# Kernel tuning notes

Measured on AMD Instinct MI355X. Metric: run time of the kernel, lower is better.

The kernel has to match this reference:

```python
import jax, jax.numpy as jnp
import numpy as np
import math

B, N, D, H, O = 2, 1024, 256, 4, 8
DT, STEPS = 0.1, 5


def setup_inputs() -> dict:
    key = jax.random.key(0)
    ks = jax.random.split(key, 8)
    inv_d = 1.0 / math.sqrt(D)
    inv_ho = 1.0 / math.sqrt(H * O)
    return {
        "x": jax.random.normal(ks[0], (B, N, D), jnp.float32),
        "Wq": jax.random.normal(ks[1], (D, D), jnp.float32) * inv_d,
        "Wk": jax.random.normal(ks[2], (D, D), jnp.float32) * inv_d,
        "Wp": jax.random.normal(ks[3], (H * O, D), jnp.float32) * inv_d,
        "bp": jnp.zeros((H * O,), jnp.float32),
        "Wo": jax.random.normal(ks[4], (D, H * O), jnp.float32) * inv_ho,
        "bo": jnp.zeros((D,), jnp.float32),
        "omega": jax.random.normal(ks[5], (H, O), jnp.float32) * 0.1,
        "coupling_scale": jnp.asarray(1.0, jnp.float32),
    }


def reference(x, Wq, Wk, Wp, bp, Wo, bo, omega, coupling_scale):
    dk = D // H
    # attention coupling J_ij = softmax(q_i.k_j / sqrt(d_k))  -> (B,H,N,N)
    q = (x @ Wq.T).reshape(B, N, H, dk).transpose(0, 2, 1, 3)
    k = (x @ Wk.T).reshape(B, N, H, dk).transpose(0, 2, 1, 3)
    J = jax.nn.softmax(jnp.einsum('bhid,bhjd->bhij', q, k) / math.sqrt(dk), axis=-1)
    # initial phases (B,H,N,O)
    phases = (x @ Wp.T + bp).reshape(B, N, H, O).transpose(0, 2, 1, 3)
    om = omega[None, :, None, :]  # (1,H,1,O)

    def step(ph, _):
        # sum_j J_ij sin(phi_j - phi_i) = cos(phi_i)*(J@sin phi) - sin(phi_i)*(J@cos phi)
        s, c = jnp.sin(ph), jnp.cos(ph)
        coupling = c * jnp.einsum('bhij,bhjo->bhio', J, s) - s * jnp.einsum('bhij,bhjo->bhio', J, c)
        new = ph + DT * (om + coupling_scale * coupling)
        new = jnp.remainder(new + jnp.pi, 2 * jnp.pi) - jnp.pi
        return new, None

    phases, _ = jax.lax.scan(step, phases, None, length=STEPS)
    sig = jnp.cos(phases).transpose(0, 2, 1, 3).reshape(B, N, H * O)
    return sig @ Wo.T + bo
```

## Files before the change

kernel.cpp:

```cpp
#include <hip/hip_runtime.h>
#include <hip/hip_bf16.h>
#include <math.h>


#define NB 1024
#define NH 4
#define DD 256
#define NO 8
#define SCSZ 131072
#define PI_F      3.14159265358979323846f
#define TWO_PI_F  6.28318530717958647692f
#define INV_2PI_F 0.15915494309189533577f

typedef __attribute__((ext_vector_type(8))) short bf16x8;
typedef __attribute__((ext_vector_type(4))) float f32x4;
typedef unsigned long long u64;

__device__ __forceinline__ float b2f_u(unsigned short s) {
    union { unsigned u; float f; } x; x.u = ((unsigned)s) << 16; return x.f;
}
__device__ __forceinline__ unsigned short f2b(float f) {
    union { float f; unsigned u; } v; v.f = f;
    unsigned r = v.u + 0x7FFFu + ((v.u >> 16) & 1u);
    return (unsigned short)(r >> 16);
}
template<bool F32>
__device__ __forceinline__ uint4 load_pack8(const void* p, size_t off) {
    if (!F32) return *(const uint4*)((const unsigned short*)p + off);
    const float* fp = (const float*)p + off;
    float4 a = *(const float4*)fp;
    float4 b = *(const float4*)(fp + 4);
    uint4 r;
    r.x = (unsigned)f2b(a.x) | ((unsigned)f2b(a.y) << 16);
    r.y = (unsigned)f2b(a.z) | ((unsigned)f2b(a.w) << 16);
    r.z = (unsigned)f2b(b.x) | ((unsigned)f2b(b.y) << 16);
    r.w = (unsigned)f2b(b.z) | ((unsigned)f2b(b.w) << 16);
    return r;
}
__device__ __forceinline__ void load8_rt(int f32, const void* p, int i, float* f) {
    if (f32) {
        const float* fp = (const float*)p + i;
        float4 a = *(const float4*)fp;
        float4 b = *(const float4*)(fp + 4);
        f[0]=a.x; f[1]=a.y; f[2]=a.z; f[3]=a.w;
        f[4]=b.x; f[5]=b.y; f[6]=b.z; f[7]=b.w;
    } else {
        uint4 u = *(const uint4*)((const unsigned short*)p + i);
        f[0] = b2f_u(u.x & 0xFFFFu); f[1] = b2f_u(u.x >> 16);
        f[2] = b2f_u(u.y & 0xFFFFu); f[3] = b2f_u(u.y >> 16);
        f[4] = b2f_u(u.z & 0xFFFFu); f[5] = b2f_u(u.z >> 16);
        f[6] = b2f_u(u.w & 0xFFFFu); f[7] = b2f_u(u.w >> 16);
    }
}
__device__ __forceinline__ float read_cs_bf16(const void* p) {
    float vb = b2f_u(*(const unsigned short*)p);
    bool ok = isfinite(vb) && fabsf(vb) > 1e-30f && fabsf(vb) < 1e30f;
    if (ok) return vb;
    return *(const float*)p;
}
__device__ __forceinline__ int detect_inline(const unsigned short* x) {
    int l = threadIdx.x & 63;
    float a0 = fabsf(b2f_u(x[2 * l]));
    float a1 = fabsf(b2f_u(x[2 * (l + 64)]));
    unsigned long long b0 = __ballot(!(a0 >= 1e-10f && a0 <= 100.0f));
    unsigned long long b1 = __ballot(!(a1 >= 1e-10f && a1 <= 100.0f));
    return (__popcll(b0) + __popcll(b1)) > 16;
}
__device__ __forceinline__ void st8_llc(void* p, u64 v) {
    __hip_atomic_store((u64*)p, v, __ATOMIC_RELAXED, __HIP_MEMORY_SCOPE_AGENT);
}
__device__ __forceinline__ void wait_ctr(unsigned int* c, unsigned target) {
    unsigned spins = 0;
    while (__hip_atomic_load(c, __ATOMIC_RELAXED, __HIP_MEMORY_SCOPE_AGENT) < target) {
        __builtin_amdgcn_s_sleep(8);
        if (++spins > (1u << 18)) break;
    }
}

template<bool F32>
__device__ void projm_impl(
    const void* __restrict__ x, const void* __restrict__ Wq,
    const void* __restrict__ Wk, const void* __restrict__ Wp,
    const void* __restrict__ bp,
    unsigned short* __restrict__ Qb, unsigned short* __restrict__ Kb,
    float* __restrict__ PH, unsigned short* __restrict__ SC)
{
    __shared__ uint4 Xsh[64 * 32];
    __shared__ uint4 Wsh[64 * 32];
    const int tid = threadIdx.x;
    const int ftile = blockIdx.x % 9, itile = blockIdx.x / 9;
    const int i0 = itile * 64, f0 = ftile * 64;
    const int wave = tid >> 6, lane = tid & 63;
    const int n = lane & 15, quad = lane >> 4;

    #pragma unroll
    for (int g = 0; g < 8; g++) {
        int fidx = g * 256 + tid;
        int row = fidx >> 5, q = fidx & 31;
        int sw = (q & 24) | ((q ^ row) & 7);
        Xsh[row * 32 + sw] = load_pack8<F32>(x, (size_t)(i0 + row) * 256 + q * 8);
        int wr = f0 + row;
        uint4 wv = make_uint4(0, 0, 0, 0);
        if (wr < 256)      wv = load_pack8<F32>(Wq, (size_t)wr * 256 + q * 8);
        else if (wr < 512) wv = load_pack8<F32>(Wk, (size_t)(wr - 256) * 256 + q * 8);
        else if (wr < 544) wv = load_pack8<F32>(Wp, (size_t)(wr - 512) * 256 + q * 8);
        Wsh[row * 32 + sw] = wv;
    }
    __syncthreads();

    f32x4 acc[4];
    #pragma unroll
    for (int s = 0; s < 4; s++) acc[s] = (f32x4){0.f, 0.f, 0.f, 0.f};
    const int xrow = wave * 16 + n;
    #pragma unroll
    for (int s = 0; s < 8; s++) {
        int qc = s * 4 + quad;
        bf16x8 b = ((const bf16x8*)Xsh)[xrow * 32 + ((qc & 24) | ((qc ^ xrow) & 7))];
        #pragma unroll
        for (int sub = 0; sub < 4; sub++) {
            int wr = sub * 16 + n;
            bf16x8 a = ((const bf16x8*)Wsh)[wr * 32 + ((qc & 24) | ((qc ^ wr) & 7))];
            acc[sub] = __builtin_amdgcn_mfma_f32_16x16x32_bf16(a, b, acc[sub], 0, 0, 0);
        }
    }

    const int ig = i0 + wave * 16 + n;
    const int bb = ig >> 10, nr = ig & 1023;
    if (ftile < 4) {
        #pragma unroll
        for (int sub = 0; sub < 4; sub++) {
            int dd = sub * 16 + quad * 4;
            ushort4 v = make_ushort4(f2b(acc[sub][0] * 0.125f), f2b(acc[sub][1] * 0.125f),
                                     f2b(acc[sub][2] * 0.125f), f2b(acc[sub][3] * 0.125f));
            *(ushort4*)(Qb + ((size_t)((bb * NH + ftile) * NB + nr)) * 64 + dd) = v;
        }
    } else if (ftile < 8) {
        int h = ftile - 4;
        #pragma unroll
        for (int sub = 0; sub < 4; sub++) {
            int dd = sub * 16 + quad * 4;
            ushort4 v = make_ushort4(f2b(acc[sub][0]), f2b(acc[sub][1]),
                                     f2b(acc[sub][2]), f2b(acc[sub][3]));
            *(ushort4*)(Kb + ((size_t)((bb * NH + h) * NB + nr)) * 64 + dd) = v;
        }
    } else {
        #pragma unroll
        for (int sub = 0; sub < 2; sub++) {
            #pragma unroll
            for (int r = 0; r < 4; r++) {
                int fp = sub * 16 + quad * 4 + r;
                int h2 = fp >> 3, o = fp & 7;
                float bpv = F32 ? ((const float*)bp)[fp]
                                : b2f_u(((const unsigned short*)bp)[fp]);
                float v = acc[sub][r] + bpv;
                int bh = bb * NH + h2;
                PH[(size_t)bh * 8192 + o * 1024 + nr] = v;
                float sv, cv;
                __sincosf(v, &sv, &cv);
                SC[(size_t)(bh * 16 + o) * 1024 + nr]     = f2b(sv);
                SC[(size_t)(bh * 16 + 8 + o) * 1024 + nr] = f2b(cv);
            }
        }
    }
}

__global__ __launch_bounds__(256) void k_projm(
    const unsigned short* x, const void* Wq, const void* Wk, const void* Wp,
    const void* bp, unsigned short* Qb, unsigned short* Kb, float* PH,
    unsigned short* SC, unsigned int* ctr)
{
    if (blockIdx.x == 0) {
        #pragma unroll
        for (int i = 0; i < 5; i++) ctr[threadIdx.x + 256 * i] = 0u;
    }
    if (detect_inline(x)) projm_impl<true >(x, Wq, Wk, Wp, bp, Qb, Kb, PH, SC);
    else                  projm_impl<false>(x, Wq, Wk, Wp, bp, Qb, Kb, PH, SC);
}

__global__ __launch_bounds__(256) void k_mega4(
    const unsigned short* __restrict__ xraw,
    const unsigned short* __restrict__ Qb, const unsigned short* __restrict__ Kb,
    const float* __restrict__ PH0,
    unsigned short* __restrict__ SCB,
    const void* __restrict__ omega, const void* __restrict__ csp,
    const void* __restrict__ Wo, const void* __restrict__ bo,
    void* __restrict__ out, unsigned int* __restrict__ ctr)
{
    __shared__ uint4 Ush[16 * 128];
    __shared__ f32x4 red[4][64];
    __shared__ float redS[4][16];
    __shared__ float Rsh[16];
    __shared__ float sig[4][32];

    const int tid = threadIdx.x;
    const int bid = blockIdx.x;
    const int bh  = bid >> 6;
    const int i0  = (bid & 63) * 16;
    const int wave = tid >> 6, lane = tid & 63;
    const int n = lane & 15, quad = lane >> 4;
    const int f32 = detect_inline(xraw);

    const unsigned short* qrow = Qb + ((size_t)(bh * NB) + i0 + n) * 64;
    bf16x8 bq0 = *(const bf16x8*)(qrow + quad * 8);
    bf16x8 bq1 = *(const bf16x8*)(qrow + 32 + quad * 8);
    float s = 0.f;
    const unsigned short* kbase = Kb + ((size_t)(bh * NB) + n) * 64;
    #pragma unroll
    for (int t = 0; t < 16; t++) {
        int jt = wave * 16 + t;
        const unsigned short* arow = kbase + (size_t)jt * 16 * 64;
        bf16x8 a0 = *(const bf16x8*)(arow + quad * 8);
        bf16x8 a1 = *(const bf16x8*)(arow + 32 + quad * 8);
        f32x4 acc = {0.f, 0.f, 0.f, 0.f};
        acc = __builtin_amdgcn_mfma_f32_16x16x32_bf16(a0, bq0, acc, 0, 0, 0);
        acc = __builtin_amdgcn_mfma_f32_16x16x32_bf16(a1, bq1, acc, 0, 0, 0);
        float u0 = __expf(acc[0]);
        float u1 = __expf(acc[1]);
        float u2 = __expf(acc[2]);
        float u3 = __expf(acc[3]);
        s += (u0 + u1) + (u2 + u3);
        ushort4 uv = make_ushort4(f2b(u0), f2b(u1), f2b(u2), f2b(u3));
        int cw = 2 * jt + (quad >> 1);
        ((ushort4*)Ush)[(n * 128 + (cw ^ (n & 7))) * 2 + (quad & 1)] = uv;
    }
    s += __shfl_xor(s, 16);
    s += __shfl_xor(s, 32);
    if (lane < 16) redS[wave][lane] = s;
    __syncthreads();
    if (tid < 16)
        Rsh[tid] = 1.0f / (redS[0][tid] + redS[1][tid] + redS[2][tid] + redS[3][tid]);

    float P[4];
    float cs_ = 0.f, om_ = 0.f;
    if (wave == 0 && n < 8) {
        const int o = n, h = bh & 3;
        cs_ = f32 ? *(const float*)csp : read_cs_bf16(csp);
        om_ = f32 ? ((const float*)omega)[h * NO + o]
                  : b2f_u(((const unsigned short*)omega)[h * NO + o]);
        float4 pv = *(const float4*)(PH0 + (size_t)bh * 8192 + o * 1024 + i0 + quad * 4);
        P[0] = pv.x; P[1] = pv.y; P[2] = pv.z; P[3] = pv.w;
    }

    #pragma unroll 1
    for (int k = 0; k < 5; k++) {
        const unsigned short* scrow = SCB + (size_t)k * SCSZ + (size_t)(bh * 16 + n) * 1024;
        unsigned short* scout       = SCB + (size_t)(k + 1) * SCSZ;
        f32x4 acc = {0.f, 0.f, 0.f, 0.f};
        #pragma unroll
        for (int t = 0; t < 8; t++) {
            int it = wave * 8 + t;
            bf16x8 a = ((const bf16x8*)Ush)[n * 128 + ((it * 4 + quad) ^ (n & 7))];
            bf16x8 b = *(const bf16x8*)(scrow + it * 32 + quad * 8);
            acc = __builtin_amdgcn_mfma_f32_16x16x32_bf16(a, b, acc, 0, 0, 0);
        }
        red[wave][lane] = acc;
        __syncthreads();

        if (wave == 0) {
            f32x4 a0 = red[0][lane], a1 = red[1][lane];
            f32x4 a2 = red[2][lane], a3 = red[3][lane];
            #pragma unroll
            for (int v = 0; v < 4; v++) acc[v] = (a0[v] + a1[v]) + (a2[v] + a3[v]);
            float C0 = __shfl_xor(acc[0], 8);
            float C1 = __shfl_xor(acc[1], 8);
            float C2 = __shfl_xor(acc[2], 8);
            float C3 = __shfl_xor(acc[3], 8);
            if (n < 8) {
                const int o = n;
                float S[4] = {acc[0], acc[1], acc[2], acc[3]};
                float C[4] = {C0, C1, C2, C3};
                float Rr[4] = {Rsh[quad * 4], Rsh[quad * 4 + 1],
                               Rsh[quad * 4 + 2], Rsh[quad * 4 + 3]};
                unsigned short sb[4], cb[4];
                #pragma unroll
                for (int r = 0; r < 4; r++) {
                    float si, ci;
                    __sincosf(P[r], &si, &ci);
                    float coup = (ci * S[r] - si * C[r]) * Rr[r];
                    float v = P[r] + 0.1f * (om_ + cs_ * coup);
                    float t2 = v + PI_F;
                    t2 -= floorf(t2 * INV_2PI_F) * TWO_PI_F;
                    P[r] = t2 - PI_F;
                    float sn, cn;
                    __sincosf(P[r], &sn, &cn);
                    sb[r] = f2b(sn); cb[r] = f2b(cn);
                }
                u64 sv = (u64)sb[0] | ((u64)sb[1] << 16) | ((u64)sb[2] << 32) | ((u64)sb[3] << 48);
                u64 cv = (u64)cb[0] | ((u64)cb[1] << 16) | ((u64)cb[2] << 32) | ((u64)cb[3] << 48);
                int i = i0 + quad * 4;
                st8_llc(scout + (size_t)(bh * 16 + o) * 1024 + i,     sv);
                st8_llc(scout + (size_t)(bh * 16 + 8 + o) * 1024 + i, cv);
            }
        }
        __syncthreads();
        if (tid == 0) {
            unsigned int* c = &ctr[(k * 8 + bh) * 32];
            atomicAdd(c, 1u);
            if (k < 4) wait_ctr(c, 64u);
        }
        if (k == 4 && tid < 4) {
            int ob = bid >> 8;
            wait_ctr(&ctr[(4 * 8 + (ob * NH + tid)) * 32], 64u);
        }
        __syncthreads();
    }

    const unsigned short* scfin = SCB + (size_t)5 * SCSZ;
    const int ob = bid >> 8, n0 = (bid & 255) * 4;
    if (tid < 32) {
        int h = tid >> 3, o = tid & 7;
        u64 q = *(const u64*)(scfin + (size_t)((ob * NH + h) * 16 + 8 + o) * 1024 + n0);
        #pragma unroll
        for (int r = 0; r < 4; r++)
            sig[r][tid] = b2f_u((unsigned short)(q >> (16 * r)));
    }
    __syncthreads();
    float wv[32];
    #pragma unroll
    for (int d0 = 0; d0 < 32; d0 += 8) load8_rt(f32, Wo, tid * 32 + d0, wv + d0);
    const float bov = f32 ? ((const float*)bo)[tid] : b2f_u(((const unsigned short*)bo)[tid]);
    #pragma unroll
    for (int r = 0; r < 4; r++) {
        float acc = bov;
        #pragma unroll
        for (int t = 0; t < 32; t++) acc += sig[r][t] * wv[t];
        size_t oi = ((size_t)ob * 1024 + n0 + r) * DD + tid;
        if (f32) ((float*)out)[oi] = acc;
        else     ((unsigned short*)out)[oi] = f2b(acc);
    }
}

extern "C" void kernel_launch(void* const* d_in, const int* in_sizes, int n_in,
                              void* d_out, int out_size, void* d_ws, size_t ws_size,
                              hipStream_t stream)
{
    const unsigned short* x = (const unsigned short*)d_in[0];
    const void* Wq  = d_in[1];
    const void* Wk  = d_in[2];
    const void* Wp  = d_in[3];
    const void* bp  = d_in[4];
    const void* Wo  = d_in[5];
    const void* bo  = d_in[6];
    const void* om  = d_in[7];
    const void* cs  = d_in[8];

    char* w = (char*)d_ws;
    unsigned short* Qb  = (unsigned short*)w;
    unsigned short* Kb  = (unsigned short*)(w + (1u << 20));
    float*          PH0 = (float*)(w + (2u << 20));
    unsigned short* SCB = (unsigned short*)(w + (2u << 20) + (256u << 10));
    unsigned int*   ctr = (unsigned int*)(w + (4u << 20));

    k_projm<<<288, 256, 0, stream>>>(x, Wq, Wk, Wp, bp, Qb, Kb, PH0, SCB, ctr);
    k_mega4<<<512, 256, 0, stream>>>(x, Qb, Kb, PH0, SCB, om, cs,
                                     Wo, bo, d_out, ctr);
}
```

Before: 122.2 us.

## Replace counter barriers with per-data flag polling on nonzero bf16 values

Removes the per-step atomic counter grid barrier. Consumers instead poll the sin/cos buffer slots directly until they become nonzero. Producers force every bf16 value to be nonzero so zero can mean 'not yet written', and the projection kernel zeroes the later step buffers up front. Each block then waits only on the exact data it needs rather than on all 64 blocks, at the cost of extra zeroing traffic, a tiny perturbation of exact-zero values, and reliance on relaxed-ordering visibility of 8-byte stores.

```diff
diff --git a/kernel.cpp b/kernel.cpp
--- a/kernel.cpp
+++ b/kernel.cpp
@@ -23,6 +23,11 @@
     union { float f; unsigned u; } v; v.f = f;
     unsigned r = v.u + 0x7FFFu + ((v.u >> 16) & 1u);
     return (unsigned short)(r >> 16);
+}
+__device__ __forceinline__ unsigned short f2b_nz(float f) {
+    unsigned short u = f2b(f);
+    if ((u & 0x7FFFu) == 0u) u |= 1u;
+    return u;
 }
 template<bool F32>
 __device__ __forceinline__ uint4 load_pack8(const void* p, size_t off) {
@@ -69,12 +74,21 @@
 __device__ __forceinline__ void st8_llc(void* p, u64 v) {
     __hip_atomic_store((u64*)p, v, __ATOMIC_RELAXED, __HIP_MEMORY_SCOPE_AGENT);
 }
-__device__ __forceinline__ void wait_ctr(unsigned int* c, unsigned target) {
-    unsigned spins = 0;
-    while (__hip_atomic_load(c, __ATOMIC_RELAXED, __HIP_MEMORY_SCOPE_AGENT) < target) {
-        __builtin_amdgcn_s_sleep(8);
-        if (++spins > (1u << 18)) break;
-    }
+__device__ __forceinline__ u64 poll_g(const void* p) {
+    u64 g; unsigned spins = 0;
+    for (;;) {
+        g = __hip_atomic_load((const u64*)p, __ATOMIC_RELAXED,
+                              __HIP_MEMORY_SCOPE_AGENT);
+        if (g) break;
+        __builtin_amdgcn_s_sleep(1);
+        if (++spins > (1u << 17)) break;
+    }
+    return g;
+}
+__device__ __forceinline__ void barrier_lds() {
+    asm volatile("s_waitcnt lgkmcnt(0)" ::: "memory");
+    __builtin_amdgcn_s_barrier();
+    __builtin_amdgcn_sched_barrier(0);
 }
 
 template<bool F32>
@@ -157,8 +171,8 @@
                 PH[(size_t)bh * 8192 + o * 1024 + nr] = v;
                 float sv, cv;
                 __sincosf(v, &sv, &cv);
-                SC[(size_t)(bh * 16 + o) * 1024 + nr]     = f2b(sv);
-                SC[(size_t)(bh * 16 + 8 + o) * 1024 + nr] = f2b(cv);
+                SC[(size_t)(bh * 16 + o) * 1024 + nr]     = f2b_nz(sv);
+                SC[(size_t)(bh * 16 + 8 + o) * 1024 + nr] = f2b_nz(cv);
             }
         }
     }
@@ -167,11 +181,13 @@
 __global__ __launch_bounds__(256) void k_projm(
     const unsigned short* x, const void* Wq, const void* Wk, const void* Wp,
     const void* bp, unsigned short* Qb, unsigned short* Kb, float* PH,
-    unsigned short* SC, unsigned int* ctr)
+    unsigned short* SC)
 {
-    if (blockIdx.x == 0) {
-        #pragma unroll
-        for (int i = 0; i < 5; i++) ctr[threadIdx.x + 256 * i] = 0u;
+    {
+        uint4* zb = (uint4*)(SC + SCSZ);
+        const unsigned stride = gridDim.x * 256u;
+        for (unsigned idx = blockIdx.x * 256u + threadIdx.x; idx < 81920u; idx += stride)
+            zb[idx] = make_uint4(0u, 0u, 0u, 0u);
     }
     if (detect_inline(x)) projm_impl<true >(x, Wq, Wk, Wp, bp, Qb, Kb, PH, SC);
     else                  projm_impl<false>(x, Wq, Wk, Wp, bp, Qb, Kb, PH, SC);
@@ -184,7 +200,7 @@
     unsigned short* __restrict__ SCB,
     const void* __restrict__ omega, const void* __restrict__ csp,
     const void* __restrict__ Wo, const void* __restrict__ bo,
-    void* __restrict__ out, unsigned int* __restrict__ ctr)
+    void* __restrict__ out)
 {
     __shared__ uint4 Ush[16 * 128];
     __shared__ f32x4 red[4][64];
@@ -245,16 +261,48 @@
     for (int k = 0; k < 5; k++) {
         const unsigned short* scrow = SCB + (size_t)k * SCSZ + (size_t)(bh * 16 + n) * 1024;
         unsigned short* scout       = SCB + (size_t)(k + 1) * SCSZ;
+
+        uint4 f[8];
+        #pragma unroll
+        for (int t = 0; t < 8; t++)
+            f[t] = *(const uint4*)(scrow + (wave * 8 + t) * 32 + quad * 8);
+
+        {
+            unsigned spins = 0;
+            for (;;) {
+                unsigned pending = 0;
+                #pragma unroll
+                for (int t = 0; t < 8; t++) {
+                    const unsigned short* fp = scrow + (wave * 8 + t) * 32 + quad * 8;
+                    if ((f[t].x | f[t].y) == 0u) {
+                        u64 g = __hip_atomic_load((const u64*)fp, __ATOMIC_RELAXED,
+                                                  __HIP_MEMORY_SCOPE_AGENT);
+                        f[t].x = (unsigned)g; f[t].y = (unsigned)(g >> 32);
+                        if (g == 0) pending = 1u;
+                    }
+                    if ((f[t].z | f[t].w) == 0u) {
+                        u64 g = __hip_atomic_load((const u64*)(fp + 4), __ATOMIC_RELAXED,
+                                                  __HIP_MEMORY_SCOPE_AGENT);
+                        f[t].z = (unsigned)g; f[t].w = (unsigned)(g >> 32);
+                        if (g == 0) pending = 1u;
+                    }
+                }
+                if (!pending) break;
+                __builtin_amdgcn_s_sleep(1);
+                if (++spins > (1u << 17)) break;
+            }
+        }
+
         f32x4 acc = {0.f, 0.f, 0.f, 0.f};
         #pragma unroll
         for (int t = 0; t < 8; t++) {
             int it = wave * 8 + t;
             bf16x8 a = ((const bf16x8*)Ush)[n * 128 + ((it * 4 + quad) ^ (n & 7))];
-            bf16x8 b = *(const bf16x8*)(scrow + it * 32 + quad * 8);
-            acc = __builtin_amdgcn_mfma_f32_16x16x32_bf16(a, b, acc, 0, 0, 0);
+            union { uint4 u; bf16x8 b; } cvt; cvt.u = f[t];
+            acc = __builtin_amdgcn_mfma_f32_16x16x32_bf16(a, cvt.b, acc, 0, 0, 0);
         }
         red[wave][lane] = acc;
-        __syncthreads();
+        barrier_lds();
 
         if (wave == 0) {
             f32x4 a0 = red[0][lane], a1 = red[1][lane];
@@ -283,7 +331,7 @@
                     P[r] = t2 - PI_F;
                     float sn, cn;
                     __sincosf(P[r], &sn, &cn);
-                    sb[r] = f2b(sn); cb[r] = f2b(cn);
+                    sb[r] = f2b_nz(sn); cb[r] = f2b_nz(cn);
                 }
                 u64 sv = (u64)sb[0] | ((u64)sb[1] << 16) | ((u64)sb[2] << 32) | ((u64)sb[3] << 48);
                 u64 cv = (u64)cb[0] | ((u64)cb[1] << 16) | ((u64)cb[2] << 32) | ((u64)cb[3] << 48);
@@ -292,24 +340,16 @@
                 st8_llc(scout + (size_t)(bh * 16 + 8 + o) * 1024 + i, cv);
             }
         }
-        __syncthreads();
-        if (tid == 0) {
-            unsigned int* c = &ctr[(k * 8 + bh) * 32];
-            atomicAdd(c, 1u);
-            if (k < 4) wait_ctr(c, 64u);
-        }
-        if (k == 4 && tid < 4) {
-            int ob = bid >> 8;
-            wait_ctr(&ctr[(4 * 8 + (ob * NH + tid)) * 32], 64u);
-        }
-        __syncthreads();
+        barrier_lds();
     }
 
     const unsigned short* scfin = SCB + (size_t)5 * SCSZ;
     const int ob = bid >> 8, n0 = (bid & 255) * 4;
     if (tid < 32) {
         int h = tid >> 3, o = tid & 7;
-        u64 q = *(const u64*)(scfin + (size_t)((ob * NH + h) * 16 + 8 + o) * 1024 + n0);
+        const u64* gp = (const u64*)(scfin + (size_t)((ob * NH + h) * 16 + 8 + o) * 1024 + n0);
+        u64 q = *gp;
+        if (q == 0) q = poll_g(gp);
         #pragma unroll
         for (int r = 0; r < 4; r++)
             sig[r][tid] = b2f_u((unsigned short)(q >> (16 * r)));
@@ -349,9 +389,8 @@
     unsigned short* Kb  = (unsigned short*)(w + (1u << 20));
     float*          PH0 = (float*)(w + (2u << 20));
     unsigned short* SCB = (unsigned short*)(w + (2u << 20) + (256u << 10));
-    unsigned int*   ctr = (unsigned int*)(w + (4u << 20));
-
-    k_projm<<<288, 256, 0, stream>>>(x, Wq, Wk, Wp, bp, Qb, Kb, PH0, SCB, ctr);
+
+    k_projm<<<288, 256, 0, stream>>>(x, Wq, Wk, Wp, bp, Qb, Kb, PH0, SCB);
     k_mega4<<<512, 256, 0, stream>>>(x, Qb, Kb, PH0, SCB, om, cs,
-                                     Wo, bo, d_out, ctr);
-}
+                                     Wo, bo, d_out);
+}
```

After: 132.6 us. 8.5% more time.

## Replace atomic-counter grid sync with per-step kernel launches

Applied to the files above, without the earlier changes.

The persistent kernel that spin-waited on global atomic counters between oscillator steps is split into five separate step launches plus a final output-projection kernel. Stream ordering now provides the cross-block synchronisation, and phases are written back to global memory between steps. This removes the spin-wait barriers and the counter reset. In exchange, each step launch recomputes the QK softmax tile and pays its own launch overhead. The block-to-head mapping is also interleaved.

```diff
diff --git a/kernel.cpp b/kernel.cpp
--- a/kernel.cpp
+++ b/kernel.cpp
@@ -65,16 +65,6 @@
     unsigned long long b0 = __ballot(!(a0 >= 1e-10f && a0 <= 100.0f));
     unsigned long long b1 = __ballot(!(a1 >= 1e-10f && a1 <= 100.0f));
     return (__popcll(b0) + __popcll(b1)) > 16;
-}
-__device__ __forceinline__ void st8_llc(void* p, u64 v) {
-    __hip_atomic_store((u64*)p, v, __ATOMIC_RELAXED, __HIP_MEMORY_SCOPE_AGENT);
-}
-__device__ __forceinline__ void wait_ctr(unsigned int* c, unsigned target) {
-    unsigned spins = 0;
-    while (__hip_atomic_load(c, __ATOMIC_RELAXED, __HIP_MEMORY_SCOPE_AGENT) < target) {
-        __builtin_amdgcn_s_sleep(8);
-        if (++spins > (1u << 18)) break;
-    }
 }
 
 template<bool F32>
@@ -167,35 +157,29 @@
 __global__ __launch_bounds__(256) void k_projm(
     const unsigned short* x, const void* Wq, const void* Wk, const void* Wp,
     const void* bp, unsigned short* Qb, unsigned short* Kb, float* PH,
-    unsigned short* SC, unsigned int* ctr)
-{
-    if (blockIdx.x == 0) {
-        #pragma unroll
-        for (int i = 0; i < 5; i++) ctr[threadIdx.x + 256 * i] = 0u;
-    }
+    unsigned short* SC)
+{
     if (detect_inline(x)) projm_impl<true >(x, Wq, Wk, Wp, bp, Qb, Kb, PH, SC);
     else                  projm_impl<false>(x, Wq, Wk, Wp, bp, Qb, Kb, PH, SC);
 }
 
-__global__ __launch_bounds__(256) void k_mega4(
+__global__ __launch_bounds__(256) void k_step(
     const unsigned short* __restrict__ xraw,
     const unsigned short* __restrict__ Qb, const unsigned short* __restrict__ Kb,
-    const float* __restrict__ PH0,
+    float* __restrict__ PH,
     unsigned short* __restrict__ SCB,
     const void* __restrict__ omega, const void* __restrict__ csp,
-    const void* __restrict__ Wo, const void* __restrict__ bo,
-    void* __restrict__ out, unsigned int* __restrict__ ctr)
+    int k)
 {
     __shared__ uint4 Ush[16 * 128];
     __shared__ f32x4 red[4][64];
     __shared__ float redS[4][16];
     __shared__ float Rsh[16];
-    __shared__ float sig[4][32];
 
     const int tid = threadIdx.x;
     const int bid = blockIdx.x;
-    const int bh  = bid >> 6;
-    const int i0  = (bid & 63) * 16;
+    const int bh  = bid & 7;
+    const int i0  = (bid >> 3) * 16;
     const int wave = tid >> 6, lane = tid & 63;
     const int n = lane & 15, quad = lane >> 4;
     const int f32 = detect_inline(xraw);
@@ -237,73 +221,73 @@
         cs_ = f32 ? *(const float*)csp : read_cs_bf16(csp);
         om_ = f32 ? ((const float*)omega)[h * NO + o]
                   : b2f_u(((const unsigned short*)omega)[h * NO + o]);
-        float4 pv = *(const float4*)(PH0 + (size_t)bh * 8192 + o * 1024 + i0 + quad * 4);
+        float4 pv = *(const float4*)(PH + (size_t)bh * 8192 + o * 1024 + i0 + quad * 4);
         P[0] = pv.x; P[1] = pv.y; P[2] = pv.z; P[3] = pv.w;
     }
 
-    #pragma unroll 1
-    for (int k = 0; k < 5; k++) {
-        const unsigned short* scrow = SCB + (size_t)k * SCSZ + (size_t)(bh * 16 + n) * 1024;
-        unsigned short* scout       = SCB + (size_t)(k + 1) * SCSZ;
-        f32x4 acc = {0.f, 0.f, 0.f, 0.f};
-        #pragma unroll
-        for (int t = 0; t < 8; t++) {
-            int it = wave * 8 + t;
-            bf16x8 a = ((const bf16x8*)Ush)[n * 128 + ((it * 4 + quad) ^ (n & 7))];
-            bf16x8 b = *(const bf16x8*)(scrow + it * 32 + quad * 8);
-            acc = __builtin_amdgcn_mfma_f32_16x16x32_bf16(a, b, acc, 0, 0, 0);
-        }
-        red[wave][lane] = acc;
-        __syncthreads();
-
-        if (wave == 0) {
-            f32x4 a0 = red[0][lane], a1 = red[1][lane];
-            f32x4 a2 = red[2][lane], a3 = red[3][lane];
+    const unsigned short* scrow = SCB + (size_t)k * SCSZ + (size_t)(bh * 16 + n) * 1024;
+    unsigned short* scout       = SCB + (size_t)(k + 1) * SCSZ;
+    f32x4 acc = {0.f, 0.f, 0.f, 0.f};
+    #pragma unroll
+    for (int t = 0; t < 8; t++) {
+        int it = wave * 8 + t;
+        bf16x8 a = ((const bf16x8*)Ush)[n * 128 + ((it * 4 + quad) ^ (n & 7))];
+        bf16x8 b = *(const bf16x8*)(scrow + it * 32 + quad * 8);
+        acc = __builtin_amdgcn_mfma_f32_16x16x32_bf16(a, b, acc, 0, 0, 0);
+    }
+    red[wave][lane] = acc;
+    __syncthreads();
+
+    if (wave == 0) {
+        f32x4 a0 = red[0][lane], a1 = red[1][lane];
+        f32x4 a2 = red[2][lane], a3 = red[3][lane];
+        #pragma unroll
+        for (int v = 0; v < 4; v++) acc[v] = (a0[v] + a1[v]) + (a2[v] + a3[v]);
+        float C0 = __shfl_xor(acc[0], 8);
+        float C1 = __shfl_xor(acc[1], 8);
+        float C2 = __shfl_xor(acc[2], 8);
+        float C3 = __shfl_xor(acc[3], 8);
+        if (n < 8) {
+            const int o = n;
+            float S[4] = {acc[0], acc[1], acc[2], acc[3]};
+            float C[4] = {C0, C1, C2, C3};
+            float Rr[4] = {Rsh[quad * 4], Rsh[quad * 4 + 1],
+                           Rsh[quad * 4 + 2], Rsh[quad * 4 + 3]};
+            unsigned short sb[4], cb[4];
             #pragma unroll
-            for (int v = 0; v < 4; v++) acc[v] = (a0[v] + a1[v]) + (a2[v] + a3[v]);
-            float C0 = __shfl_xor(acc[0], 8);
-            float C1 = __shfl_xor(acc[1], 8);
-            float C2 = __shfl_xor(acc[2], 8);
-            float C3 = __shfl_xor(acc[3], 8);
-            if (n < 8) {
-                const int o = n;
-                float S[4] = {acc[0], acc[1], acc[2], acc[3]};
-                float C[4] = {C0, C1, C2, C3};
-                float Rr[4] = {Rsh[quad * 4], Rsh[quad * 4 + 1],
-                               Rsh[quad * 4 + 2], Rsh[quad * 4 + 3]};
-                unsigned short sb[4], cb[4];
-                #pragma unroll
-                for (int r = 0; r < 4; r++) {
-                    float si, ci;
-                    __sincosf(P[r], &si, &ci);
-                    float coup = (ci * S[r] - si * C[r]) * Rr[r];
-                    float v = P[r] + 0.1f * (om_ + cs_ * coup);
-                    float t2 = v + PI_F;
-                    t2 -= floorf(t2 * INV_2PI_F) * TWO_PI_F;
-                    P[r] = t2 - PI_F;
-                    float sn, cn;
-                    __sincosf(P[r], &sn, &cn);
-                    sb[r] = f2b(sn); cb[r] = f2b(cn);
-                }
-                u64 sv = (u64)sb[0] | ((u64)sb[1] << 16) | ((u64)sb[2] << 32) | ((u64)sb[3] << 48);
-                u64 cv = (u64)cb[0] | ((u64)cb[1] << 16) | ((u64)cb[2] << 32) | ((u64)cb[3] << 48);
-                int i = i0 + quad * 4;
-                st8_llc(scout + (size_t)(bh * 16 + o) * 1024 + i,     sv);
-                st8_llc(scout + (size_t)(bh * 16 + 8 + o) * 1024 + i, cv);
+            for (int r = 0; r < 4; r++) {
+                float si, ci;
+                __sincosf(P[r], &si, &ci);
+                float coup = (ci * S[r] - si * C[r]) * Rr[r];
+                float v = P[r] + 0.1f * (om_ + cs_ * coup);
+                float t2 = v + PI_F;
+                t2 -= floorf(t2 * INV_2PI_F) * TWO_PI_F;
+                P[r] = t2 - PI_F;
+                float sn, cn;
+                __sincosf(P[r], &sn, &cn);
+                sb[r] = f2b(sn); cb[r] = f2b(cn);
             }
-        }
-        __syncthreads();
-        if (tid == 0) {
-            unsigned int* c = &ctr[(k * 8 + bh) * 32];
-            atomicAdd(c, 1u);
-            if (k < 4) wait_ctr(c, 64u);
-        }
-        if (k == 4 && tid < 4) {
-            int ob = bid >> 8;
-            wait_ctr(&ctr[(4 * 8 + (ob * NH + tid)) * 32], 64u);
-        }
-        __syncthreads();
-    }
+            u64 sv = (u64)sb[0] | ((u64)sb[1] << 16) | ((u64)sb[2] << 32) | ((u64)sb[3] << 48);
+            u64 cv = (u64)cb[0] | ((u64)cb[1] << 16) | ((u64)cb[2] << 32) | ((u64)cb[3] << 48);
+            int i = i0 + quad * 4;
+            *(u64*)(scout + (size_t)(bh * 16 + o) * 1024 + i)     = sv;
+            *(u64*)(scout + (size_t)(bh * 16 + 8 + o) * 1024 + i) = cv;
+            *(float4*)(PH + (size_t)bh * 8192 + o * 1024 + i) =
+                make_float4(P[0], P[1], P[2], P[3]);
+        }
+    }
+}
+
+__global__ __launch_bounds__(256) void k_out(
+    const unsigned short* __restrict__ xraw,
+    const unsigned short* __restrict__ SCB,
+    const void* __restrict__ Wo, const void* __restrict__ bo,
+    void* __restrict__ out)
+{
+    __shared__ float sig[4][32];
+    const int tid = threadIdx.x;
+    const int bid = blockIdx.x;
+    const int f32 = detect_inline(xraw);
 
     const unsigned short* scfin = SCB + (size_t)5 * SCSZ;
     const int ob = bid >> 8, n0 = (bid & 255) * 4;
@@ -349,9 +333,9 @@
     unsigned short* Kb  = (unsigned short*)(w + (1u << 20));
     float*          PH0 = (float*)(w + (2u << 20));
     unsigned short* SCB = (unsigned short*)(w + (2u << 20) + (256u << 10));
-    unsigned int*   ctr = (unsigned int*)(w + (4u << 20));
-
-    k_projm<<<288, 256, 0, stream>>>(x, Wq, Wk, Wp, bp, Qb, Kb, PH0, SCB, ctr);
-    k_mega4<<<512, 256, 0, stream>>>(x, Qb, Kb, PH0, SCB, om, cs,
-                                     Wo, bo, d_out, ctr);
-}
+
+    k_projm<<<288, 256, 0, stream>>>(x, Wq, Wk, Wp, bp, Qb, Kb, PH0, SCB);
+    for (int k = 0; k < 5; k++)
+        k_step<<<512, 256, 0, stream>>>(x, Qb, Kb, PH0, SCB, om, cs, k);
+    k_out<<<512, 256, 0, stream>>>(x, SCB, Wo, bo, d_out);
+}
```

Result: slower. 144.7 us (+18.4%).
